# Performance work log

Hardware: AMD Instinct MI355X
Metric: run time of the kernel (lower is better)

## Reference

```python
import jax, jax.numpy as jnp
import numpy as np

VOCAB_SIZE = 32   # embedding dim
HID = 32          # LSTMCell units = RNN_SIZE // 2
RNN_SIZE = 64
CARD_EMBED_SIZE = 64

B, P, L = 2048, 64, 16
VOCAB_COUNT = 10000


def setup_inputs() -> dict:
    key = jax.random.key(0)
    ks = jax.random.split(key, 7)
    x = jax.random.randint(ks[0], (B, P, L), 0, VOCAB_COUNT, dtype=jnp.int32)
    embed_table = jax.random.normal(ks[1], (VOCAB_COUNT, VOCAB_SIZE), dtype=jnp.float32) * 0.05
    # Keras LSTM gate layout: [i, f, c(g), o] concatenated along last axis
    Wk = jax.random.normal(ks[2], (VOCAB_SIZE, 4 * HID), dtype=jnp.float32) * 0.1
    Wr = jax.random.normal(ks[3], (HID, 4 * HID), dtype=jnp.float32) * 0.1
    b = jax.random.normal(ks[4], (4 * HID,), dtype=jnp.float32) * 0.01
    Wd = jax.random.normal(ks[5], (P * RNN_SIZE, CARD_EMBED_SIZE), dtype=jnp.float32) * 0.02
    bd = jnp.zeros((CARD_EMBED_SIZE,), dtype=jnp.float32)
    return {"x": x, "embed_table": embed_table, "Wk": Wk, "Wr": Wr, "b": b,
            "Wd": Wd, "bd": bd}


def _lstm_last_h(emb, mask, Wk, Wr, b):
    """emb: [N, T, D]; mask: [N, T] bool. Returns final hidden state [N, HID].
    Masked timesteps (token 0, Keras mask_zero=True) leave the state unchanged."""
    N = emb.shape[0]
    emb_t = jnp.swapaxes(emb, 0, 1)    # [T, N, D]
    mask_t = jnp.swapaxes(mask, 0, 1)  # [T, N]

    def step(carry, xm):
        h, c = carry
        xt, mt = xm
        z = xt @ Wk + h @ Wr + b                       # [N, 4H]
        i, f, g, o = jnp.split(z, 4, axis=-1)
        i = jax.nn.sigmoid(i)
        f = jax.nn.sigmoid(f)
        g = jnp.tanh(g)
        o = jax.nn.sigmoid(o)
        c_new = f * c + i * g
        h_new = o * jnp.tanh(c_new)
        m = mt[:, None]
        return (jnp.where(m, h_new, h), jnp.where(m, c_new, c)), None

    h0 = jnp.zeros((N, HID), dtype=emb.dtype)
    (h, _), _ = jax.lax.scan(step, (h0, h0), (emb_t, mask_t))
    return h


def reference(x, embed_table, Wk, Wr, b, Wd, bd):
    Bq, Pq, Lq = x.shape
    flat_x = x.reshape(Bq * Pq, Lq)                       # [N, T]
    emb = embed_table[flat_x]                             # [N, T, 32]
    mask = flat_x != 0                                    # mask_zero=True
    # forward direction
    h_fw = _lstm_last_h(emb, mask, Wk, Wr, b)
    # backward direction (go_backwards=True): reverse sequence and mask; same cell weights
    h_bw = _lstm_last_h(emb[:, ::-1, :], mask[:, ::-1], Wk, Wr, b)
    state = jnp.concatenate([h_fw, h_bw], axis=-1)        # [N, 64]
    concated = state.reshape(Bq, Pq * RNN_SIZE)           # [B, P*64]
    # max_path_length * RNN_SIZE != CARD_EMBED_SIZE -> dense branch
    return jnp.tanh(concated @ Wd + bd)
```

## Files before the change

### kernel.cpp

```cpp
#include <hip/hip_runtime.h>

typedef _Float16 half8_t __attribute__((ext_vector_type(8)));
typedef __fp16   fp16x2_t __attribute__((ext_vector_type(2)));
typedef float    f32x4_t __attribute__((ext_vector_type(4)));
typedef unsigned int u32x4_t __attribute__((ext_vector_type(4)));

static constexpr int BATCH = 2048;
static constexpr int NSEQ  = BATCH * 64;
static constexpr int VOCABN = 10000;
static constexpr float L2E = 1.44269504f;

__global__ __launch_bounds__(256) void prep_all(const float* __restrict__ emb,
                                                const float* __restrict__ Wr,
                                                const float* __restrict__ Wk,
                                                const float* __restrict__ Wd,
                                                const float* __restrict__ bias,
                                                ushort* __restrict__ zxt16,
                                                ushort* __restrict__ fwr,
                                                ushort* __restrict__ fwd) {
    const int bid = blockIdx.x, tid = threadIdx.x;
    if (bid < 5000) {
        const int v = bid * 2 + (tid >> 7);
        const int row = tid & 127;
        const int b = row >> 4, grp = (row & 15) >> 2, r = row & 3;
        const float* er = emb + v * 32;
        float a = bias[row];
        #pragma unroll
        for (int d = 0; d < 32; ++d) a = fmaf(er[d], Wk[d * 128 + row], a);
        const float s = (b == 4 || b == 5) ? (2.f * L2E) : (-L2E);
        _Float16 hv = (_Float16)(a * s);
        zxt16[v * 128 + grp * 32 + b * 4 + r] = __builtin_bit_cast(ushort, hv);
    } else if (bid < 5008) {
        if (tid >= 64) return;
        const int lane = tid;
        const int b = bid - 5000;
        const float s = (b == 4 || b == 5) ? (2.f * L2E) : (-L2E);
        #pragma unroll
        for (int j = 0; j < 8; ++j) {
            int kk = (lane >> 4) * 8 + j;
            int krow = 4 * (kk >> 3) + (kk & 3) + 16 * ((kk >> 2) & 1);
            int col = b * 16 + (lane & 15);
            _Float16 v = (_Float16)(Wr[krow * 128 + col] * s);
            fwr[(b * 64 + lane) * 8 + j] = __builtin_bit_cast(ushort, v);
        }
    } else {
        const int idx = (bid - 5008) * 256 + tid;
        const int lane = idx & 63, ksblk = idx >> 6;
        const int ks = ksblk >> 2, blk = ksblk & 3;
        #pragma unroll
        for (int j = 0; j < 8; ++j) {
            const int k = ks * 32 + (lane >> 4) * 8 + j;
            const int col = blk * 16 + (lane & 15);
            _Float16 v = (_Float16)Wd[k * 64 + col];
            fwd[ksblk * 512 + lane * 8 + j] = __builtin_bit_cast(ushort, v);
        }
    }
}

__global__ __launch_bounds__(256, 3) void lstm_mfma(const int* __restrict__ x,
                                                    const ushort* __restrict__ fwr,
                                                    const ushort* __restrict__ zxt16,
                                                    ushort* __restrict__ state16) {
    __shared__ int toks[16 * 32];

    const int tid = threadIdx.x, lane = tid & 63, wid = tid >> 6;
    const int i15 = lane & 15, grp = lane >> 4;
    const long blkSeq = (long)blockIdx.x * 32;

    if (tid < 128) {
        int s = tid >> 2, t4 = (tid & 3) * 4;
        int4 v = *(const int4*)(x + (blkSeq + s) * 16 + t4);
        toks[(t4 + 0) * 32 + s] = v.x; toks[(t4 + 1) * 32 + s] = v.y;
        toks[(t4 + 2) * 32 + s] = v.z; toks[(t4 + 3) * 32 + s] = v.w;
    }

    const half8_t* fwr8 = (const half8_t*)fwr;
    half8_t Awr[8];
    #pragma unroll
    for (int b = 0; b < 8; ++b) Awr[b] = fwr8[b * 64 + lane];

    __syncthreads();

    const int seqIB = wid * 8 + (i15 & 7);
    const bool bw = i15 >= 8;
    const int dstep = bw ? -32 : 32;
    int idx = (bw ? 15 * 32 : 0) + seqIB;

    float creg[4][2];
    #pragma unroll
    for (int r = 0; r < 4; ++r) creg[r][0] = creg[r][1] = 0.f;
    half8_t Bh = __builtin_bit_cast(half8_t, (u32x4_t){0u, 0u, 0u, 0u});

    int tok_cur = toks[idx]; idx += dstep;
    int tok_nx  = toks[idx]; idx += dstep;
    const half8_t* ztab = (const half8_t*)zxt16;
    half8_t zb0[4], zb1[4];
    {
        const half8_t* zr = ztab + (long)tok_cur * 16 + grp * 4;
        #pragma unroll
        for (int c = 0; c < 4; ++c) zb0[c] = zr[c];
    }

    f32x4_t acc[8];

    #pragma unroll 2
    for (int s = 0; s < 16; ++s) {
        const half8_t* zc = (s & 1) ? zb1 : zb0;
        #pragma unroll
        for (int b = 0; b < 8; ++b) {
            const int c = b >> 1, o4 = (b & 1) * 4;
            f32x4_t cc = { (float)zc[c][o4 + 0], (float)zc[c][o4 + 1],
                           (float)zc[c][o4 + 2], (float)zc[c][o4 + 3] };
            acc[b] = __builtin_amdgcn_mfma_f32_16x16x32_f16(Awr[b], Bh, cc, 0, 0, 0);
        }
        if (s < 15) {
            const half8_t* zr = ztab + (long)tok_nx * 16 + grp * 4;
            if (s & 1) {
                #pragma unroll
                for (int c = 0; c < 4; ++c) zb0[c] = zr[c];
            } else {
                #pragma unroll
                for (int c = 0; c < 4; ++c) zb1[c] = zr[c];
            }
        }
        const bool m = (tok_cur != 0);
        u32x4_t w;
        #pragma unroll
        for (int hf = 0; hf < 2; ++hf) {
            float hn[4];
            #pragma unroll
            for (int r = 0; r < 4; ++r) {
                float Ei = __builtin_amdgcn_exp2f(acc[0 + hf][r]);
                float Ef = __builtin_amdgcn_exp2f(acc[2 + hf][r]);
                float Eg = __builtin_amdgcn_exp2f(acc[4 + hf][r]);
                float Eo = __builtin_amdgcn_exp2f(acc[6 + hf][r]);
                float D1 = 1.f + Ef;
                float D2 = (1.f + Ei) * (1.f + Eg);
                float num = fmaf(creg[r][hf], D2, (Eg - 1.f) * D1);
                float cn  = num * __builtin_amdgcn_rcpf(D1 * D2);
                float Ec  = __builtin_amdgcn_exp2f(cn * (2.f * L2E));
                float roc = __builtin_amdgcn_rcpf((1.f + Eo) * (1.f + Ec));
                hn[r] = (Ec - 1.f) * roc;
                creg[r][hf] = m ? cn : creg[r][hf];
            }
            fp16x2_t pa = __builtin_amdgcn_cvt_pkrtz(hn[0], hn[1]);
            fp16x2_t pb = __builtin_amdgcn_cvt_pkrtz(hn[2], hn[3]);
            if (hf == 0) { w.x = __builtin_bit_cast(unsigned int, pa);
                           w.y = __builtin_bit_cast(unsigned int, pb); }
            else         { w.z = __builtin_bit_cast(unsigned int, pa);
                           w.w = __builtin_bit_cast(unsigned int, pb); }
        }
        half8_t Bh_new = __builtin_bit_cast(half8_t, w);
        Bh = m ? Bh_new : Bh;
        tok_cur = tok_nx;
        if (s < 14) { tok_nx = toks[idx]; idx += dstep; }
    }

    {
        u32x4_t wv = __builtin_bit_cast(u32x4_t, Bh);
        ushort* base = state16 + (blkSeq + seqIB) * 64 + (bw ? 32 : 0);
        uint2 lo = {wv.x, wv.y}, hi = {wv.z, wv.w};
        *(uint2*)(base + 4 * grp) = lo;
        *(uint2*)(base + 16 + 4 * grp) = hi;
    }
}

__global__ __launch_bounds__(256) void proj_mfma(const ushort* __restrict__ state16,
                                                 const ushort* __restrict__ fwd,
                                                 const float* __restrict__ bd,
                                                 float* __restrict__ out) {
    const int tid = threadIdx.x, lane = tid & 63, wid = tid >> 6;
    const int i15 = lane & 15, grp = lane >> 4;
    const int r0 = blockIdx.x * 16;

    const half8_t* fw8 = (const half8_t*)fwd;
    const half8_t* sa  = (const half8_t*)state16;

    float cinit = bd[wid * 16 + i15];
    f32x4_t acc = {cinit, cinit, cinit, cinit};

    const int abase = (r0 + i15) * 512 + grp;
    #pragma unroll 4
    for (int ks = 0; ks < 128; ++ks) {
        half8_t A = sa[abase + ks * 4];
        acc = __builtin_amdgcn_mfma_f32_16x16x32_f16(A, fw8[(ks * 4 + wid) * 64 + lane],
                                                     acc, 0, 0, 0);
    }

    #pragma unroll
    for (int q = 0; q < 4; ++q) {
        float e = __builtin_amdgcn_exp2f(acc[q] * (2.f * L2E));
        float t = fmaf(-2.f, __builtin_amdgcn_rcpf(1.f + e), 1.f);
        out[(r0 + grp * 4 + q) * 64 + wid * 16 + i15] = t;
    }
}

extern "C" void kernel_launch(void* const* d_in, const int* in_sizes, int n_in,
                              void* d_out, int out_size, void* d_ws, size_t ws_size,
                              hipStream_t stream) {
    const int*   x    = (const int*)d_in[0];
    const float* emb  = (const float*)d_in[1];
    const float* Wk   = (const float*)d_in[2];
    const float* Wr   = (const float*)d_in[3];
    const float* bias = (const float*)d_in[4];
    const float* Wd   = (const float*)d_in[5];
    const float* bd   = (const float*)d_in[6];
    float* out = (float*)d_out;

    ushort* state16 = (ushort*)d_ws;
    ushort* zxt16   = (ushort*)((char*)d_ws + 16777216);
    ushort* fwr     = (ushort*)((char*)d_ws + 19337216);
    ushort* fwd     = (ushort*)((char*)d_ws + 19345408);

    prep_all<<<5136, 256, 0, stream>>>(emb, Wr, Wk, Wd, bias, zxt16, fwr, fwd);
    lstm_mfma<<<NSEQ / 32, 256, 0, stream>>>(x, fwr, zxt16, state16);
    proj_mfma<<<BATCH / 16, 256, 0, stream>>>(state16, fwd, bd, out);
}
```

Before: 178.6 us.

## Stage recurrent weights in LDS and split gate MFMAs into two halves

Moves the recurrent weight fragments out of VGPRs into shared memory and re-reads them from LDS each step. The asm barrier on the offset keeps the compiler from hoisting those loads back into registers. The eight MFMAs are split into two groups of four, and the first group's activations are computed before the second group is issued, which shrinks the live accumulators. Together these cut register pressure so launch bounds can ask for four blocks per SM instead of three, at the cost of extra LDS reads on the serial recurrence path.

Measured after the change: 172.3 us. 3.5% less time.

```diff
diff --git a/kernel.cpp b/kernel.cpp
--- a/kernel.cpp
+++ b/kernel.cpp
@@ -57,11 +57,12 @@
     }
 }
 
-__global__ __launch_bounds__(256, 3) void lstm_mfma(const int* __restrict__ x,
+__global__ __launch_bounds__(256, 4) void lstm_mfma(const int* __restrict__ x,
                                                     const ushort* __restrict__ fwr,
                                                     const ushort* __restrict__ zxt16,
                                                     ushort* __restrict__ state16) {
     __shared__ int toks[16 * 32];
+    __shared__ half8_t awr_lds[8 * 64];
 
     const int tid = threadIdx.x, lane = tid & 63, wid = tid >> 6;
     const int i15 = lane & 15, grp = lane >> 4;
@@ -73,12 +74,11 @@
         toks[(t4 + 0) * 32 + s] = v.x; toks[(t4 + 1) * 32 + s] = v.y;
         toks[(t4 + 2) * 32 + s] = v.z; toks[(t4 + 3) * 32 + s] = v.w;
     }
-
-    const half8_t* fwr8 = (const half8_t*)fwr;
-    half8_t Awr[8];
-    #pragma unroll
-    for (int b = 0; b < 8; ++b) Awr[b] = fwr8[b * 64 + lane];
-
+    {
+        const half8_t* fwr8 = (const half8_t*)fwr;
+        awr_lds[tid]       = fwr8[tid];
+        awr_lds[tid + 256] = fwr8[tid + 256];
+    }
     __syncthreads();
 
     const int seqIB = wid * 8 + (i15 & 7);
@@ -101,17 +101,22 @@
         for (int c = 0; c < 4; ++c) zb0[c] = zr[c];
     }
 
-    f32x4_t acc[8];
+    unsigned awr_off = 0;
 
     #pragma unroll 2
     for (int s = 0; s < 16; ++s) {
+        asm volatile("" : "+v"(awr_off));
+        const half8_t* Aw = (const half8_t*)((const char*)awr_lds + awr_off) + lane;
         const half8_t* zc = (s & 1) ? zb1 : zb0;
-        #pragma unroll
-        for (int b = 0; b < 8; ++b) {
-            const int c = b >> 1, o4 = (b & 1) * 4;
-            f32x4_t cc = { (float)zc[c][o4 + 0], (float)zc[c][o4 + 1],
-                           (float)zc[c][o4 + 2], (float)zc[c][o4 + 3] };
-            acc[b] = __builtin_amdgcn_mfma_f32_16x16x32_f16(Awr[b], Bh, cc, 0, 0, 0);
+        const bool m = (tok_cur != 0);
+        u32x4_t w;
+
+        f32x4_t acce[4];
+        #pragma unroll
+        for (int k = 0; k < 4; ++k) {
+            f32x4_t cc = { (float)zc[k][0], (float)zc[k][1],
+                           (float)zc[k][2], (float)zc[k][3] };
+            acce[k] = __builtin_amdgcn_mfma_f32_16x16x32_f16(Aw[(2 * k) * 64], Bh, cc, 0, 0, 0);
         }
         if (s < 15) {
             const half8_t* zr = ztab + (long)tok_nx * 16 + grp * 4;
@@ -123,32 +128,56 @@
                 for (int c = 0; c < 4; ++c) zb1[c] = zr[c];
             }
         }
-        const bool m = (tok_cur != 0);
-        u32x4_t w;
-        #pragma unroll
-        for (int hf = 0; hf < 2; ++hf) {
+        {
             float hn[4];
             #pragma unroll
             for (int r = 0; r < 4; ++r) {
-                float Ei = __builtin_amdgcn_exp2f(acc[0 + hf][r]);
-                float Ef = __builtin_amdgcn_exp2f(acc[2 + hf][r]);
-                float Eg = __builtin_amdgcn_exp2f(acc[4 + hf][r]);
-                float Eo = __builtin_amdgcn_exp2f(acc[6 + hf][r]);
+                float Ei = __builtin_amdgcn_exp2f(acce[0][r]);
+                float Ef = __builtin_amdgcn_exp2f(acce[1][r]);
+                float Eg = __builtin_amdgcn_exp2f(acce[2][r]);
+                float Eo = __builtin_amdgcn_exp2f(acce[3][r]);
                 float D1 = 1.f + Ef;
                 float D2 = (1.f + Ei) * (1.f + Eg);
-                float num = fmaf(creg[r][hf], D2, (Eg - 1.f) * D1);
+                float num = fmaf(creg[r][0], D2, (Eg - 1.f) * D1);
                 float cn  = num * __builtin_amdgcn_rcpf(D1 * D2);
                 float Ec  = __builtin_amdgcn_exp2f(cn * (2.f * L2E));
                 float roc = __builtin_amdgcn_rcpf((1.f + Eo) * (1.f + Ec));
                 hn[r] = (Ec - 1.f) * roc;
-                creg[r][hf] = m ? cn : creg[r][hf];
+                creg[r][0] = m ? cn : creg[r][0];
             }
             fp16x2_t pa = __builtin_amdgcn_cvt_pkrtz(hn[0], hn[1]);
             fp16x2_t pb = __builtin_amdgcn_cvt_pkrtz(hn[2], hn[3]);
-            if (hf == 0) { w.x = __builtin_bit_cast(unsigned int, pa);
-                           w.y = __builtin_bit_cast(unsigned int, pb); }
-            else         { w.z = __builtin_bit_cast(unsigned int, pa);
-                           w.w = __builtin_bit_cast(unsigned int, pb); }
+            w.x = __builtin_bit_cast(unsigned int, pa);
+            w.y = __builtin_bit_cast(unsigned int, pb);
+        }
+        f32x4_t acco[4];
+        #pragma unroll
+        for (int k = 0; k < 4; ++k) {
+            f32x4_t cc = { (float)zc[k][4], (float)zc[k][5],
+                           (float)zc[k][6], (float)zc[k][7] };
+            acco[k] = __builtin_amdgcn_mfma_f32_16x16x32_f16(Aw[(2 * k + 1) * 64], Bh, cc, 0, 0, 0);
+        }
+        {
+            float hn[4];
+            #pragma unroll
+            for (int r = 0; r < 4; ++r) {
+                float Ei = __builtin_amdgcn_exp2f(acco[0][r]);
+                float Ef = __builtin_amdgcn_exp2f(acco[1][r]);
+                float Eg = __builtin_amdgcn_exp2f(acco[2][r]);
+                float Eo = __builtin_amdgcn_exp2f(acco[3][r]);
+                float D1 = 1.f + Ef;
+                float D2 = (1.f + Ei) * (1.f + Eg);
+                float num = fmaf(creg[r][1], D2, (Eg - 1.f) * D1);
+                float cn  = num * __builtin_amdgcn_rcpf(D1 * D2);
+                float Ec  = __builtin_amdgcn_exp2f(cn * (2.f * L2E));
+                float roc = __builtin_amdgcn_rcpf((1.f + Eo) * (1.f + Ec));
+                hn[r] = (Ec - 1.f) * roc;
+                creg[r][1] = m ? cn : creg[r][1];
+            }
+            fp16x2_t pa = __builtin_amdgcn_cvt_pkrtz(hn[0], hn[1]);
+            fp16x2_t pb = __builtin_amdgcn_cvt_pkrtz(hn[2], hn[3]);
+            w.z = __builtin_bit_cast(unsigned int, pa);
+            w.w = __builtin_bit_cast(unsigned int, pb);
         }
         half8_t Bh_new = __builtin_bit_cast(half8_t, w);
         Bh = m ? Bh_new : Bh;
```
